# Performance work log

Measured on AMD Instinct MI355X. Metric: run time of the kernel, lower is better.

The kernel has to match this reference:

```python
import jax, jax.numpy as jnp
import numpy as np

NEG_SLOPE = 0.1
BN_EPS = 1e-5

def lrelu(z):
    return jax.nn.leaky_relu(z, NEG_SLOPE)

def conv1d(x, w, b):
    # x: [B,C,L], w: [O,I,K], 'same' padding for K=3
    y = jax.lax.conv_general_dilated(x, w, (1,), [(1, 1)], dimension_numbers=('NCH', 'OIH', 'NCH'))
    return y + b[None, :, None]

def batchnorm_train(x, g, be):
    # training-mode BatchNorm1d over (B, L) per channel; x: [B,C,L]
    m = x.mean(axis=(0, 2), keepdims=True)
    v = x.var(axis=(0, 2), keepdims=True)
    return g[None, :, None] * (x - m) * jax.lax.rsqrt(v + BN_EPS) + be[None, :, None]

def setup_inputs() -> dict:
    key = jax.random.key(0)
    ks = jax.random.split(key, 16)
    L, B, E = 100, 32, 512
    F, K, M, H, DEC = 256, 3, 128, 512, 512
    D = F + 2  # cnn feats + 2 coord dims
    s = 0.02
    inp = {
        'x': jax.random.normal(ks[0], (L, B, E), jnp.float32),
        'h': jax.random.normal(ks[1], (B, H), jnp.float32),
        'cw1': jax.random.normal(ks[2], (F, E, K), jnp.float32) * s,
        'cb1': jnp.zeros((F,), jnp.float32),
        'g1': jnp.ones((F,), jnp.float32), 'be1': jnp.zeros((F,), jnp.float32),
        'cw2': jax.random.normal(ks[3], (F, F, K), jnp.float32) * s,
        'cb2': jnp.zeros((F,), jnp.float32),
        'g2': jnp.ones((F,), jnp.float32), 'be2': jnp.zeros((F,), jnp.float32),
        'cw3': jax.random.normal(ks[4], (F, F, K), jnp.float32) * s,
        'cb3': jnp.zeros((F,), jnp.float32),
        'g3': jnp.ones((F,), jnp.float32), 'be3': jnp.zeros((F,), jnp.float32),
        'cw4': jax.random.normal(ks[5], (F, F, K), jnp.float32) * s,
        'cb4': jnp.zeros((F,), jnp.float32),
        'g4': jnp.ones((F,), jnp.float32), 'be4': jnp.zeros((F,), jnp.float32),
        'W1': jax.random.normal(ks[6], (2 * D + H, M), jnp.float32) * s,
        'b1': jnp.zeros((M,), jnp.float32),
        'W2': jax.random.normal(ks[7], (M, M), jnp.float32) * s,
        'b2': jnp.zeros((M,), jnp.float32),
        'W3': jax.random.normal(ks[8], (M, M), jnp.float32) * s,
        'b3': jnp.zeros((M,), jnp.float32),
        'W4': jax.random.normal(ks[9], (M, M), jnp.float32) * s,
        'b4': jnp.zeros((M,), jnp.float32),
        'F1': jax.random.normal(ks[10], (M, M), jnp.float32) * s,
        'fb1': jnp.zeros((M,), jnp.float32),
        'F2': jax.random.normal(ks[11], (M, DEC), jnp.float32) * s,
        'fb2': jnp.zeros((DEC,), jnp.float32),
    }
    return inp

def reference(x, h, cw1, cb1, g1, be1, cw2, cb2, g2, be2, cw3, cb3, g3, be3,
              cw4, cb4, g4, be4, W1, b1, W2, b2, W3, b3, W4, b4, F1, fb1, F2, fb2):
    # x: [L,B,E] -> [B,E,L]
    xc = jnp.transpose(x, (1, 2, 0))
    for cw, cb, g, be in ((cw1, cb1, g1, be1), (cw2, cb2, g2, be2),
                          (cw3, cb3, g3, be3), (cw4, cb4, g4, be4)):
        xc = batchnorm_train(lrelu(conv1d(xc, cw, cb)), g, be)
    xc = jnp.transpose(xc, (0, 2, 1))  # [B,L,F]
    B, L, _ = xc.shape
    # coordinate tensor: cvt_coord(i, L) = [(i/sqrt(L)-2)/2, (i%sqrt(L)-2)/2]
    i = jnp.arange(L, dtype=jnp.float32)
    sL = jnp.sqrt(jnp.float32(L))
    coord = jnp.stack([(i / sL - 2.0) / 2.0, (jnp.mod(i, sL) - 2.0) / 2.0], axis=-1)
    xf = jnp.concatenate([xc, jnp.broadcast_to(coord, (B, L, 2))], axis=-1)  # [B,L,D]
    D = xf.shape[-1]
    # pair[b,i,j] = [xf[b,j], xf[b,i], h[b]]; split W1 to avoid materializing concat
    Wa, Wb, Wc = W1[:D], W1[D:2 * D], W1[2 * D:]
    A = xf @ Wa                              # contribution of x_j, [B,L,M]
    C = xf @ Wb + (h @ Wc + b1)[:, None, :]  # contribution of x_i and h, [B,L,M]
    g = lrelu(C[:, :, None, :] + A[:, None, :, :])  # [B,L,L,M]
    g = lrelu(g @ W2 + b2)
    g = lrelu(g @ W3 + b3)
    g = lrelu(g @ W4 + b4)
    s = g.sum(axis=(1, 2))  # sum-pool over all L*L pairs -> [B,M]
    out = lrelu(lrelu(s @ F1 + fb1) @ F2 + fb2)  # [B,dec_hid]
    return out
```

## Files before the change

### kernel.cpp

```cpp
#include <hip/hip_runtime.h>
#include <hip/hip_bf16.h>
#include <stdint.h>
#include <stddef.h>

#define NEG 0.1f

typedef __attribute__((ext_vector_type(8))) short short8;
typedef __attribute__((ext_vector_type(16))) float floatx16;

__device__ __forceinline__ unsigned f2bf(float f) {
  union { float f; unsigned u; } v; v.f = f;
  unsigned r = v.u + 0x7FFFu + ((v.u >> 16) & 1u);
  return r >> 16;
}
__device__ __forceinline__ unsigned pk2bf(float a, float b) {
  __hip_bfloat162 hh = __float22bfloat162_rn(make_float2(a, b));
  union { __hip_bfloat162 h; unsigned u; } v; v.h = hh; return v.u;
}
__device__ __forceinline__ float bits2f(unsigned u) {
  union { unsigned u; float f; } v; v.u = u; return v.f;
}

__global__ void k_prep(const float* __restrict__ cw1, const float* __restrict__ cw2,
                       const float* __restrict__ cw3, const float* __restrict__ cw4,
                       unsigned short* __restrict__ wt1, unsigned short* __restrict__ wt2,
                       unsigned short* __restrict__ wt3, unsigned short* __restrict__ wt4,
                       const float* __restrict__ W1, unsigned short* __restrict__ wab,
                       const float* __restrict__ W2, const float* __restrict__ W3,
                       const float* __restrict__ W4, unsigned short* __restrict__ wmlp,
                       const float* __restrict__ h, float* __restrict__ hc) {
  __shared__ float tile[64 * 65];
  int bid = blockIdx.x, tid = threadIdx.x;
  if (bid < 1280) {
    int z = bid;
    int E; const float* cw; unsigned short* wt;
    if (z < 512) { E = 512; cw = cw1; wt = wt1; }
    else {
      int q = (z - 512) >> 8; E = 256;
      cw = (q == 0) ? cw2 : ((q == 1) ? cw3 : cw4);
      wt = (q == 0) ? wt2 : ((q == 1) ? wt3 : wt4);
      z = (z - 512) & 255;
    }
    int idx = z * 256 + tid;
    int f = idx / E, e = idx - f * E;
    const float* s = cw + (size_t)idx * 3;
    unsigned short* d = wt + (size_t)f * 3 * E + e;
    d[0] = (unsigned short)f2bf(s[0]);
    d[E] = (unsigned short)f2bf(s[1]);
    d[2 * E] = (unsigned short)f2bf(s[2]);
  } else if (bid < 1304) {
    int tw = bid - 1280;
    int half = tw / 12, rem = tw % 12, dt = rem >> 1, nt = rem & 1;
    int c = tid & 63, rq = tid >> 6;
#pragma unroll
    for (int it = 0; it < 16; ++it) {
      int r = rq + it * 4;
      int kp = dt * 64 + r;
      float v = 0.f;
      if (kp < 258) v = W1[(size_t)(half * 258 + kp) * 128 + nt * 64 + c];
      tile[r * 65 + c] = v;
    }
    __syncthreads();
#pragma unroll
    for (int it = 0; it < 16; ++it) {
      int r2 = rq + it * 4;
      wab[(size_t)(half * 128 + nt * 64 + r2) * 384 + dt * 64 + c] =
          (unsigned short)f2bf(tile[c * 65 + r2]);
    }
  } else if (bid < 1496) {
    int i2 = (bid - 1304) * 256 + tid;
    int n = i2 & 127, k = (i2 >> 7) & 127, zz = i2 >> 14;
    const float* W = (zz == 0) ? W2 : ((zz == 1) ? W3 : W4);
    float v = W[k * 128 + n];
    int w = n >> 5, l = ((k >> 3) & 1) * 32 + (n & 31), kk = k >> 4, j = k & 7;
    int i = (((zz * 4 + w) * 8 + kk) << 9) | (l << 3) | j;
    wmlp[i] = (unsigned short)f2bf(v);
  } else {
    int t = bid - 1496;
    int b = t >> 2, seg = t & 3;
    int m = tid & 127, sub = tid >> 7;
    int k0 = seg * 128 + sub * 64;
    const float* hr = h + b * 512 + k0;
    const float* Wc = W1 + (size_t)(516 + k0) * 128 + m;
    float a0 = 0.f, a1 = 0.f, a2 = 0.f, a3 = 0.f, a4 = 0.f, a5 = 0.f, a6 = 0.f, a7 = 0.f;
#pragma unroll
    for (int k = 0; k < 64; k += 8) {
      a0 += hr[k + 0] * Wc[(size_t)(k + 0) * 128];
      a1 += hr[k + 1] * Wc[(size_t)(k + 1) * 128];
      a2 += hr[k + 2] * Wc[(size_t)(k + 2) * 128];
      a3 += hr[k + 3] * Wc[(size_t)(k + 3) * 128];
      a4 += hr[k + 4] * Wc[(size_t)(k + 4) * 128];
      a5 += hr[k + 5] * Wc[(size_t)(k + 5) * 128];
      a6 += hr[k + 6] * Wc[(size_t)(k + 6) * 128];
      a7 += hr[k + 7] * Wc[(size_t)(k + 7) * 128];
    }
    float s = ((a0 + a1) + (a2 + a3)) + ((a4 + a5) + (a6 + a7));
    atomicAdd(&hc[b * 128 + m], s);
  }
}

__global__ __launch_bounds__(256, 2) void k_conv(
    const float* __restrict__ zin, const float* __restrict__ bnin,
    const float* __restrict__ gamv, const float* __restrict__ betv,
    const unsigned short* __restrict__ wt, const float* __restrict__ cb,
    float* __restrict__ zout, float* __restrict__ bnout, int E, int xmode) {
  extern __shared__ unsigned short smem[];
  const int SL = (E == 512) ? 520 : 264;
  unsigned short* slab = smem;
  unsigned short* Bs = smem + 34 * SL;
  const int K = 3 * E, NC = K >> 6, NCH = NC >> 1;
  const int esh = (E == 512) ? 9 : 8;
  int tid = threadIdx.x;
  int lane = tid & 63, wave = tid >> 6;
  int khalf = wave >> 1, cwave = wave & 1;
  int r0 = blockIdx.x * 32, ct = blockIdx.y;
  int i32 = lane & 31;
  int koff = (lane >> 5) << 3;

  int lrow = (r0 + i32) % 100;
  bool vks0 = (lrow >= 1), vks2 = (lrow <= 98);

  if (xmode) {
    for (int s = wave; s < 34; s += 4) {
      int m = r0 - 1 + s; m = min(max(m, 0), 3199);
      int b = m / 100, l = m - b * 100;
      size_t base = (size_t)(l * 32 + b) * 512;
#pragma unroll
      for (int cc = 0; cc < 2; ++cc) {
        int ch = cc * 256 + lane * 4;
        float4 v = *(const float4*)(zin + base + ch);
        uint2 p; p.x = pk2bf(v.x, v.y); p.y = pk2bf(v.z, v.w);
        *(uint2*)(&slab[s * SL + ch]) = p;
      }
    }
  } else {
    const float inv = 1.f / 3200.f;
    float sc[4], sh[4];
#pragma unroll
    for (int q = 0; q < 4; ++q) {
      int ch = lane * 4 + q;
      float mme = bnin[ch] * inv;
      float var = bnin[256 + ch] * inv - mme * mme;
      sc[q] = gamv[ch] * rsqrtf(var + 1e-5f);
      sh[q] = betv[ch] - mme * sc[q];
    }
    for (int s = wave; s < 34; s += 4) {
      int m = r0 - 1 + s; m = min(max(m, 0), 3199);
      float4 v = *(const float4*)(zin + (size_t)m * 256 + lane * 4);
      uint2 p;
      p.x = pk2bf(v.x * sc[0] + sh[0], v.y * sc[1] + sh[1]);
      p.y = pk2bf(v.z * sc[2] + sh[2], v.w * sc[3] + sh[3]);
      *(uint2*)(&slab[s * SL + lane * 4]) = p;
    }
  }

  floatx16 acc;
#pragma unroll
  for (int q = 0; q < 16; ++q) acc[q] = 0.f;

  int t128 = tid & 127;
  int brow = t128 >> 1, bhalf = (t128 & 1) * 32;
  const unsigned short* wrow = wt + (size_t)(ct * 64 + brow) * K + khalf * NCH * 64 + bhalf;
  uint4 pre[4];
#pragma unroll
  for (int t = 0; t < 4; ++t) pre[t] = *(const uint4*)(wrow + t * 8);

  for (int c = 0; c < NCH; ++c) {
    unsigned short* Bc = Bs + (khalf * 2 + (c & 1)) * (64 * 72);
#pragma unroll
    for (int t = 0; t < 4; ++t)
      *(uint4*)(&Bc[brow * 72 + bhalf + t * 8]) = pre[t];
    __syncthreads();
    if (c + 1 < NCH) {
#pragma unroll
      for (int t = 0; t < 4; ++t)
        pre[t] = *(const uint4*)(wrow + (c + 1) * 64 + t * 8);
    }
    int cg = khalf * NCH + c;
    int ks = (cg << 6) >> esh;
    int ebase = (cg << 6) & (E - 1);
    bool v = (ks == 0) ? vks0 : ((ks == 2) ? vks2 : true);
    int srow = i32 + ks;
#pragma unroll
    for (int kk = 0; kk < 4; ++kk) {
      short8 a = {};
      if (v) a = *(const short8*)(&slab[srow * SL + ebase + kk * 16 + koff]);
      short8 b8 = *(const short8*)(&Bc[(cwave * 32 + i32) * 72 + kk * 16 + koff]);
      acc = __builtin_amdgcn_mfma_f32_32x32x16_bf16(a, b8, acc, 0, 0, 0);
    }
  }

  __syncthreads();
  float* scr = (float*)smem;
  if (khalf == 1) {
#pragma unroll
    for (int reg = 0; reg < 16; ++reg) {
      int rowp = (reg & 3) + 8 * (reg >> 2) + 4 * (lane >> 5);
      scr[cwave * 1024 + rowp * 32 + i32] = acc[reg];
    }
  }
  __syncthreads();
  if (khalf == 0) {
    int f = ct * 64 + cwave * 32 + i32;
    float bias = cb[f];
    float s1 = 0.f, s2 = 0.f;
#pragma unroll
    for (int reg = 0; reg < 16; ++reg) {
      int rowp = (reg & 3) + 8 * (reg >> 2) + 4 * (lane >> 5);
      int m = r0 + rowp;
      float v = acc[reg] + scr[cwave * 1024 + rowp * 32 + i32] + bias;
      v = fmaxf(v, NEG * v);
      zout[(size_t)m * 256 + f] = v;
      s1 += v; s2 += v * v;
    }
    s1 += __shfl_xor(s1, 32, 64);
    s2 += __shfl_xor(s2, 32, 64);
    if (lane < 32) { atomicAdd(&bnout[f], s1); atomicAdd(&bnout[256 + f], s2); }
  }
}

__global__ __launch_bounds__(128, 2) void k_ac(
    const float* __restrict__ zin, const float* __restrict__ bnin,
    const float* __restrict__ gamv, const float* __restrict__ betv,
    const unsigned short* __restrict__ wab, const float* __restrict__ hc,
    const float* __restrict__ b1v,
    unsigned short* __restrict__ Abf, unsigned short* __restrict__ Cbf) {
  __shared__ unsigned short slab[32 * 328];
  __shared__ unsigned short Bs[2 * 64 * 72];
  int tid = threadIdx.x;
  int lane = tid & 63, wave = tid >> 6;
  int r0 = blockIdx.x * 32, ct = blockIdx.y;
  int i32 = lane & 31;
  int koff = (lane >> 5) << 3;
  const float inv = 1.f / 3200.f;

  {
    float sc[4], sh[4];
#pragma unroll
    for (int q = 0; q < 4; ++q) {
      int ch = lane * 4 + q;
      float mme = bnin[ch] * inv;
      float var = bnin[256 + ch] * inv - mme * mme;
      sc[q] = gamv[ch] * rsqrtf(var + 1e-5f);
      sh[q] = betv[ch] - mme * sc[q];
    }
    for (int s = wave; s < 32; s += 2) {
      int m = r0 + s;
      float4 v = *(const float4*)(zin + (size_t)m * 256 + lane * 4);
      uint2 p;
      p.x = pk2bf(v.x * sc[0] + sh[0], v.y * sc[1] + sh[1]);
      p.y = pk2bf(v.z * sc[2] + sh[2], v.w * sc[3] + sh[3]);
      *(uint2*)(&slab[s * 328 + lane * 4]) = p;
    }
    if (wave == 0) {
      int s = i32, half = (lane >> 5) * 32;
      int m = r0 + s, l = m % 100;
      float c0 = ((float)l * 0.1f - 2.0f) * 0.5f;
      float c1 = ((float)(l % 10) - 2.0f) * 0.5f;
#pragma unroll
      for (int seg = 0; seg < 4; ++seg) {
        uint4 z4; z4.x = z4.y = z4.z = z4.w = 0u;
        if (half == 0 && seg == 0) z4.x = pk2bf(c0, c1);
        *(uint4*)(&slab[s * 328 + 256 + half + seg * 8]) = z4;
      }
    }
  }

  floatx16 acc;
#pragma unroll
  for (int q = 0; q < 16; ++q) acc[q] = 0.f;

  int brow = tid >> 1, bhalf = (tid & 1) * 32;
  uint4 pre[4];
#pragma unroll
  for (int t = 0; t < 4; ++t)
    pre[t] = *(const uint4*)(wab + (size_t)(ct * 64 + brow) * 384 + bhalf + t * 8);

  for (int c = 0; c < 5; ++c) {
    unsigned short* Bc = Bs + (c & 1) * (64 * 72);
#pragma unroll
    for (int t = 0; t < 4; ++t)
      *(uint4*)(&Bc[brow * 72 + bhalf + t * 8]) = pre[t];
    __syncthreads();
    if (c + 1 < 5) {
#pragma unroll
      for (int t = 0; t < 4; ++t)
        pre[t] = *(const uint4*)(wab + (size_t)(ct * 64 + brow) * 384 + (c + 1) * 64 + bhalf + t * 8);
    }
#pragma unroll
    for (int kk = 0; kk < 4; ++kk) {
      short8 a = *(const short8*)(&slab[i32 * 328 + c * 64 + kk * 16 + koff]);
      short8 b8 = *(const short8*)(&Bc[(wave * 32 + i32) * 72 + kk * 16 + koff]);
      acc = __builtin_amdgcn_mfma_f32_32x32x16_bf16(a, b8, acc, 0, 0, 0);
    }
  }

  int n = ct * 64 + wave * 32 + i32;
#pragma unroll
  for (int reg = 0; reg < 16; ++reg) {
    int rowp = (reg & 3) + 8 * (reg >> 2) + 4 * (lane >> 5);
    int m = r0 + rowp;
    float v = acc[reg];
    if (ct < 2) {
      Abf[(size_t)m * 128 + n] = (unsigned short)f2bf(v);
    } else {
      int b = m / 100;
      int nc = n - 128;
      Cbf[(size_t)m * 128 + nc] =
          (unsigned short)f2bf(v + hc[b * 128 + nc] + b1v[nc]);
    }
  }
}

__global__ __launch_bounds__(256, 2) void k_mlp(
    const unsigned short* __restrict__ Abf, const unsigned short* __restrict__ Cbf,
    const unsigned short* __restrict__ wmlp, const float* __restrict__ b2,
    const float* __restrict__ b3, const float* __restrict__ b4,
    float* __restrict__ sout) {
  __shared__ unsigned short gs0[128 * 128];
  __shared__ unsigned short gs1[128 * 128];
  int tid = threadIdx.x, lane = tid & 63, wave = tid >> 6;
  int ln31 = lane & 31;
  int half = lane >> 5;
  int rx = ln31 & 15;

  short8 wreg[3][8];
#pragma unroll
  for (int z = 0; z < 3; ++z)
#pragma unroll
    for (int kk = 0; kk < 8; ++kk)
      wreg[z][kk] = *(const short8*)(wmlp + (size_t)(((z * 4 + wave) * 8 + kk) * 512) + lane * 8);

  int wb = wave * 32;
  float4 bq[2][4];
#pragma unroll
  for (int q = 0; q < 4; ++q) {
    bq[0][q] = *(const float4*)(b2 + wb + q * 8 + 4 * half);
    bq[1][q] = *(const float4*)(b3 + wb + q * 8 + 4 * half);
  }
  float bv4 = b4[wb + ln31];

  for (int ti = 0; ti < 2; ++ti) {
    int t = blockIdx.x + ti * 1264;
    int b = t / 79, tt = t - b * 79;
    __syncthreads();
    {
      int lr = wb + (lane >> 1);
      int hh = lane & 1;
      int lbase = lr * 128, lrx = lr & 15;
      int r = tt * 128 + lr;
      if (r > 9999) r = 9999;
      const unsigned short* Crow = Cbf + (size_t)(b * 100 + r / 100) * 128;
      const unsigned short* Arow = Abf + (size_t)(b * 100 + r % 100) * 128;
#pragma unroll
      for (int it = 0; it < 8; ++it) {
        int cc = hh * 64 + it * 8;
        uint4 c4 = *(const uint4*)(Crow + cc);
        uint4 a4 = *(const uint4*)(Arow + cc);
        unsigned cw[4] = {c4.x, c4.y, c4.z, c4.w};
        unsigned aw[4] = {a4.x, a4.y, a4.z, a4.w};
        unsigned ow[4];
#pragma unroll
        for (int q = 0; q < 4; ++q) {
          float x0 = bits2f(cw[q] << 16) + bits2f(aw[q] << 16);
          float x1 = bits2f(cw[q] & 0xFFFF0000u) + bits2f(aw[q] & 0xFFFF0000u);
          x0 = fmaxf(x0, NEG * x0);
          x1 = fmaxf(x1, NEG * x1);
          ow[q] = pk2bf(x0, x1);
        }
        uint4 o4; o4.x = ow[0]; o4.y = ow[1]; o4.z = ow[2]; o4.w = ow[3];
        *(uint4*)(&gs0[lbase + (((hh * 8 + it) ^ lrx) << 3)]) = o4;
      }
    }
    __syncthreads();

#pragma unroll
    for (int z = 0; z < 2; ++z) {
      const unsigned short* src = z ? gs1 : gs0;
      unsigned short* dst = z ? gs0 : gs1;
#pragma unroll
      for (int rg = 0; rg < 4; ++rg) {
        floatx16 acc;
#pragma unroll
        for (int q = 0; q < 16; ++q) acc[q] = 0.f;
        int rowb = (rg * 32 + ln31) * 128;
#pragma unroll
        for (int kk = 0; kk < 8; ++kk) {
          short8 g8 = *(const short8*)(&src[rowb + (((kk * 2 + half) ^ rx) << 3)]);
          acc = __builtin_amdgcn_mfma_f32_32x32x16_bf16(wreg[z][kk], g8, acc, 0, 0, 0);
        }
        int pr = rg * 32 + ln31;
        int prb = pr * 128;
#pragma unroll
        for (int q = 0; q < 4; ++q) {
          float4 bb = bq[z][q];
          float v0 = acc[q * 4 + 0] + bb.x; v0 = fmaxf(v0, NEG * v0);
          float v1 = acc[q * 4 + 1] + bb.y; v1 = fmaxf(v1, NEG * v1);
          float v2 = acc[q * 4 + 2] + bb.z; v2 = fmaxf(v2, NEG * v2);
          float v3 = acc[q * 4 + 3] + bb.w; v3 = fmaxf(v3, NEG * v3);
          uint2 p; p.x = pk2bf(v0, v1); p.y = pk2bf(v2, v3);
          *(uint2*)(&dst[prb + (((wave * 4 + q) ^ rx) << 3) + half * 4]) = p;
        }
      }
      __syncthreads();
    }

    float colsum = 0.f;
#pragma unroll
    for (int rg = 0; rg < 4; ++rg) {
      floatx16 acc;
#pragma unroll
      for (int q = 0; q < 16; ++q) acc[q] = 0.f;
      int rowb = (rg * 32 + ln31) * 128;
#pragma unroll
      for (int kk = 0; kk < 8; ++kk) {
        short8 a8 = *(const short8*)(&gs0[rowb + (((kk * 2 + half) ^ rx) << 3)]);
        acc = __builtin_amdgcn_mfma_f32_32x32x16_bf16(a8, wreg[2][kk], acc, 0, 0, 0);
      }
#pragma unroll
      for (int reg = 0; reg < 16; ++reg) {
        int rowp = (reg & 3) + 8 * (reg >> 2) + 4 * half;
        int p = tt * 128 + rg * 32 + rowp;
        float v = acc[reg] + bv4;
        v = fmaxf(v, NEG * v);
        colsum += (p < 10000) ? v : 0.f;
      }
    }
    colsum += __shfl_xor(colsum, 32, 64);
    if (lane < 32) atomicAdd(&sout[b * 128 + wb + lane], colsum);
  }
}

__global__ void k_final(const float* __restrict__ s, const float* __restrict__ F1,
                        const float* __restrict__ fb1, const float* __restrict__ F2,
                        const float* __restrict__ fb2, float* __restrict__ out) {
  __shared__ float sl[128], t1[128];
  int b = blockIdx.x, t = threadIdx.x;
  if (t < 128) sl[t] = s[b * 128 + t];
  __syncthreads();
  if (t < 128) {
    float a = fb1[t];
    for (int k = 0; k < 128; ++k) a += sl[k] * F1[k * 128 + t];
    t1[t] = fmaxf(a, NEG * a);
  }
  __syncthreads();
  for (int o = t; o < 512; o += 256) {
    float a = fb2[o];
    for (int k = 0; k < 128; ++k) a += t1[k] * F2[k * 512 + o];
    out[b * 512 + o] = fmaxf(a, NEG * a);
  }
}

extern "C" void kernel_launch(void* const* d_in, const int* in_sizes, int n_in,
                              void* d_out, int out_size, void* d_ws, size_t ws_size,
                              hipStream_t stream) {
  const float* x   = (const float*)d_in[0];
  const float* h   = (const float*)d_in[1];
  const float* cw1 = (const float*)d_in[2];
  const float* cb1 = (const float*)d_in[3];
  const float* g1  = (const float*)d_in[4];
  const float* be1 = (const float*)d_in[5];
  const float* cw2 = (const float*)d_in[6];
  const float* cb2 = (const float*)d_in[7];
  const float* g2  = (const float*)d_in[8];
  const float* be2 = (const float*)d_in[9];
  const float* cw3 = (const float*)d_in[10];
  const float* cb3 = (const float*)d_in[11];
  const float* g3  = (const float*)d_in[12];
  const float* be3 = (const float*)d_in[13];
  const float* cw4 = (const float*)d_in[14];
  const float* cb4 = (const float*)d_in[15];
  const float* g4  = (const float*)d_in[16];
  const float* be4 = (const float*)d_in[17];
  const float* W1  = (const float*)d_in[18];
  const float* b1  = (const float*)d_in[19];
  const float* W2  = (const float*)d_in[20];
  const float* b2  = (const float*)d_in[21];
  const float* W3  = (const float*)d_in[22];
  const float* b3  = (const float*)d_in[23];
  const float* W4  = (const float*)d_in[24];
  const float* b4  = (const float*)d_in[25];
  const float* F1  = (const float*)d_in[26];
  const float* fb1 = (const float*)d_in[27];
  const float* F2  = (const float*)d_in[28];
  const float* fb2 = (const float*)d_in[29];

  char* ws = (char*)d_ws;
  float* bn0  = (float*)(ws + 0);
  float* bn1  = (float*)(ws + 2048);
  float* bn2  = (float*)(ws + 4096);
  float* bn3  = (float*)(ws + 6144);
  float* sbuf = (float*)(ws + 8192);
  float* hc   = (float*)(ws + 24576);
  float* za   = (float*)(ws + 40960);
  float* zb   = (float*)(ws + 3317760);
  unsigned short* wt1  = (unsigned short*)(ws + 6594560);
  unsigned short* wt2  = (unsigned short*)(ws + 7380992);
  unsigned short* wt3  = (unsigned short*)(ws + 7774208);
  unsigned short* wt4  = (unsigned short*)(ws + 8167424);
  unsigned short* wab  = (unsigned short*)(ws + 8560640);
  unsigned short* wmlp = (unsigned short*)(ws + 8757248);
  unsigned short* Abf  = (unsigned short*)(ws + 8855552);
  unsigned short* Cbf  = (unsigned short*)(ws + 9674752);

  hipMemsetAsync(d_ws, 0, 40960, stream);

  k_prep<<<1624, 256, 0, stream>>>(cw1, cw2, cw3, cw4, wt1, wt2, wt3, wt4,
                                   W1, wab, W2, W3, W4, wmlp, h, hc);

  const int lds1 = (34 * 520 + 4 * 64 * 72) * 2;
  const int lds2 = (34 * 264 + 4 * 64 * 72) * 2;
  k_conv<<<dim3(100, 4), 256, lds1, stream>>>(x,  nullptr, nullptr, nullptr, wt1, cb1, za, bn0, 512, 1);
  k_conv<<<dim3(100, 4), 256, lds2, stream>>>(za, bn0, g1, be1, wt2, cb2, zb, bn1, 256, 0);
  k_conv<<<dim3(100, 4), 256, lds2, stream>>>(zb, bn1, g2, be2, wt3, cb3, za, bn2, 256, 0);
  k_conv<<<dim3(100, 4), 256, lds2, stream>>>(za, bn2, g3, be3, wt4, cb4, zb, bn3, 256, 0);

  k_ac<<<dim3(100, 4), 128, 0, stream>>>(zb, bn3, g4, be4, wab, hc, b1, Abf, Cbf);

  k_mlp<<<1264, 256, 0, stream>>>(Abf, Cbf, wmlp, b2, b3, b4, sbuf);
  k_final<<<32, 256, 0, stream>>>(sbuf, F1, fb1, F2, fb2, (float*)d_out);
}
```

Measured before the change: 283.6 us.

## Restructure weight prep, ping-pong MLP buffers, and split final GEMV reductions

Result: slower. 308.0 us (+8.6%).

```diff
diff --git a/kernel.cpp b/kernel.cpp
--- a/kernel.cpp
+++ b/kernel.cpp
@@ -30,27 +30,30 @@
                        const float* __restrict__ W4, unsigned short* __restrict__ wmlp,
                        const float* __restrict__ h, float* __restrict__ hc) {
   __shared__ float tile[64 * 65];
+  __shared__ unsigned short tw[1536];
   int bid = blockIdx.x, tid = threadIdx.x;
-  if (bid < 1280) {
-    int z = bid;
-    int E; const float* cw; unsigned short* wt;
-    if (z < 512) { E = 512; cw = cw1; wt = wt1; }
+  if (bid < 1024) {
+    const float* cw; unsigned short* wt; int E, f;
+    if (bid < 256) { cw = cw1; wt = wt1; E = 512; f = bid; }
     else {
-      int q = (z - 512) >> 8; E = 256;
+      int z = bid - 256; int q = z >> 8; f = z & 255; E = 256;
       cw = (q == 0) ? cw2 : ((q == 1) ? cw3 : cw4);
       wt = (q == 0) ? wt2 : ((q == 1) ? wt3 : wt4);
-      z = (z - 512) & 255;
-    }
-    int idx = z * 256 + tid;
-    int f = idx / E, e = idx - f * E;
-    const float* s = cw + (size_t)idx * 3;
-    unsigned short* d = wt + (size_t)f * 3 * E + e;
-    d[0] = (unsigned short)f2bf(s[0]);
-    d[E] = (unsigned short)f2bf(s[1]);
-    d[2 * E] = (unsigned short)f2bf(s[2]);
-  } else if (bid < 1304) {
-    int tw = bid - 1280;
-    int half = tw / 12, rem = tw % 12, dt = rem >> 1, nt = rem & 1;
+    }
+    int KE = 3 * E;
+    const float* src = cw + (size_t)f * KE;
+    for (int e = tid; e < E; e += 256) {
+      tw[e]         = (unsigned short)f2bf(src[e * 3]);
+      tw[E + e]     = (unsigned short)f2bf(src[e * 3 + 1]);
+      tw[2 * E + e] = (unsigned short)f2bf(src[e * 3 + 2]);
+    }
+    __syncthreads();
+    unsigned short* dst = wt + (size_t)f * KE;
+    int nch = KE >> 3;
+    if (tid < nch) *(uint4*)(dst + tid * 8) = *(const uint4*)(tw + tid * 8);
+  } else if (bid < 1048) {
+    int tw2 = bid - 1024;
+    int half = tw2 / 12, rem = tw2 % 12, dt = rem >> 1, nt = rem & 1;
     int c = tid & 63, rq = tid >> 6;
 #pragma unroll
     for (int it = 0; it < 16; ++it) {
@@ -67,8 +70,8 @@
       wab[(size_t)(half * 128 + nt * 64 + r2) * 384 + dt * 64 + c] =
           (unsigned short)f2bf(tile[c * 65 + r2]);
     }
-  } else if (bid < 1496) {
-    int i2 = (bid - 1304) * 256 + tid;
+  } else if (bid < 1240) {
+    int i2 = (bid - 1048) * 256 + tid;
     int n = i2 & 127, k = (i2 >> 7) & 127, zz = i2 >> 14;
     const float* W = (zz == 0) ? W2 : ((zz == 1) ? W3 : W4);
     float v = W[k * 128 + n];
@@ -76,7 +79,7 @@
     int i = (((zz * 4 + w) * 8 + kk) << 9) | (l << 3) | j;
     wmlp[i] = (unsigned short)f2bf(v);
   } else {
-    int t = bid - 1496;
+    int t = bid - 1240;
     int b = t >> 2, seg = t & 3;
     int m = tid & 127, sub = tid >> 7;
     int k0 = seg * 128 + sub * 64;
@@ -312,17 +315,105 @@
   }
 }
 
+__device__ __forceinline__ void mlp_g0(
+    unsigned short* dst, const unsigned short* __restrict__ Abf,
+    const unsigned short* __restrict__ Cbf, int b, int tt, int wave, int lane) {
+  int lr = wave * 32 + (lane >> 1);
+  int hh = lane & 1;
+  int lbase = lr * 128, lrx = lr & 15;
+  int r = tt * 128 + lr;
+  if (r > 9999) r = 9999;
+  const unsigned short* Crow = Cbf + (size_t)(b * 100 + r / 100) * 128;
+  const unsigned short* Arow = Abf + (size_t)(b * 100 + r % 100) * 128;
+#pragma unroll
+  for (int it = 0; it < 8; ++it) {
+    int cc = hh * 64 + it * 8;
+    uint4 c4 = *(const uint4*)(Crow + cc);
+    uint4 a4 = *(const uint4*)(Arow + cc);
+    unsigned cw[4] = {c4.x, c4.y, c4.z, c4.w};
+    unsigned aw[4] = {a4.x, a4.y, a4.z, a4.w};
+    unsigned ow[4];
+#pragma unroll
+    for (int q = 0; q < 4; ++q) {
+      float x0 = bits2f(cw[q] << 16) + bits2f(aw[q] << 16);
+      float x1 = bits2f(cw[q] & 0xFFFF0000u) + bits2f(aw[q] & 0xFFFF0000u);
+      x0 = fmaxf(x0, NEG * x0);
+      x1 = fmaxf(x1, NEG * x1);
+      ow[q] = pk2bf(x0, x1);
+    }
+    uint4 o4; o4.x = ow[0]; o4.y = ow[1]; o4.z = ow[2]; o4.w = ow[3];
+    *(uint4*)(&dst[lbase + (((hh * 8 + it) ^ lrx) << 3)]) = o4;
+  }
+}
+
+__device__ __forceinline__ void mlp_layerF(
+    const unsigned short* src, unsigned short* dst, const short8* wz,
+    const float4* bz, int wave, int lane) {
+  int ln31 = lane & 31, half = lane >> 5;
+  int rx = ln31 & 15;
+#pragma unroll
+  for (int rg = 0; rg < 4; ++rg) {
+    floatx16 acc;
+#pragma unroll
+    for (int q = 0; q < 16; ++q) acc[q] = 0.f;
+    int rowb = (rg * 32 + ln31) * 128;
+#pragma unroll
+    for (int kk = 0; kk < 8; ++kk) {
+      short8 g8 = *(const short8*)(&src[rowb + (((kk * 2 + half) ^ rx) << 3)]);
+      acc = __builtin_amdgcn_mfma_f32_32x32x16_bf16(wz[kk], g8, acc, 0, 0, 0);
+    }
+    int prb = (rg * 32 + ln31) * 128;
+#pragma unroll
+    for (int q = 0; q < 4; ++q) {
+      float4 bb = bz[q];
+      float v0 = acc[q * 4 + 0] + bb.x; v0 = fmaxf(v0, NEG * v0);
+      float v1 = acc[q * 4 + 1] + bb.y; v1 = fmaxf(v1, NEG * v1);
+      float v2 = acc[q * 4 + 2] + bb.z; v2 = fmaxf(v2, NEG * v2);
+      float v3 = acc[q * 4 + 3] + bb.w; v3 = fmaxf(v3, NEG * v3);
+      uint2 p; p.x = pk2bf(v0, v1); p.y = pk2bf(v2, v3);
+      *(uint2*)(&dst[prb + (((wave * 4 + q) ^ rx) << 3) + half * 4]) = p;
+    }
+  }
+}
+
+__device__ __forceinline__ float mlp_layerR(
+    const unsigned short* src, const short8* wz, float bv4, int tt, int lane) {
+  int ln31 = lane & 31, half = lane >> 5;
+  int rx = ln31 & 15;
+  float colsum = 0.f;
+#pragma unroll
+  for (int rg = 0; rg < 4; ++rg) {
+    floatx16 acc;
+#pragma unroll
+    for (int q = 0; q < 16; ++q) acc[q] = 0.f;
+    int rowb = (rg * 32 + ln31) * 128;
+#pragma unroll
+    for (int kk = 0; kk < 8; ++kk) {
+      short8 a8 = *(const short8*)(&src[rowb + (((kk * 2 + half) ^ rx) << 3)]);
+      acc = __builtin_amdgcn_mfma_f32_32x32x16_bf16(a8, wz[kk], acc, 0, 0, 0);
+    }
+#pragma unroll
+    for (int reg = 0; reg < 16; ++reg) {
+      int rowp = (reg & 3) + 8 * (reg >> 2) + 4 * half;
+      int p = tt * 128 + rg * 32 + rowp;
+      float v = acc[reg] + bv4;
+      v = fmaxf(v, NEG * v);
+      colsum += (p < 10000) ? v : 0.f;
+    }
+  }
+  return colsum;
+}
+
 __global__ __launch_bounds__(256, 2) void k_mlp(
     const unsigned short* __restrict__ Abf, const unsigned short* __restrict__ Cbf,
     const unsigned short* __restrict__ wmlp, const float* __restrict__ b2,
     const float* __restrict__ b3, const float* __restrict__ b4,
     float* __restrict__ sout) {
-  __shared__ unsigned short gs0[128 * 128];
-  __shared__ unsigned short gs1[128 * 128];
+  __shared__ unsigned short gsX[128 * 128];
+  __shared__ unsigned short gsY[128 * 128];
   int tid = threadIdx.x, lane = tid & 63, wave = tid >> 6;
-  int ln31 = lane & 31;
-  int half = lane >> 5;
-  int rx = ln31 & 15;
+  int ln31 = lane & 31, half = lane >> 5;
+  int wb = wave * 32;
 
   short8 wreg[3][8];
 #pragma unroll
@@ -331,7 +422,6 @@
     for (int kk = 0; kk < 8; ++kk)
       wreg[z][kk] = *(const short8*)(wmlp + (size_t)(((z * 4 + wave) * 8 + kk) * 512) + lane * 8);
 
-  int wb = wave * 32;
   float4 bq[2][4];
 #pragma unroll
   for (int q = 0; q < 4; ++q) {
@@ -340,113 +430,65 @@
   }
   float bv4 = b4[wb + ln31];
 
-  for (int ti = 0; ti < 2; ++ti) {
-    int t = blockIdx.x + ti * 1264;
-    int b = t / 79, tt = t - b * 79;
-    __syncthreads();
-    {
-      int lr = wb + (lane >> 1);
-      int hh = lane & 1;
-      int lbase = lr * 128, lrx = lr & 15;
-      int r = tt * 128 + lr;
-      if (r > 9999) r = 9999;
-      const unsigned short* Crow = Cbf + (size_t)(b * 100 + r / 100) * 128;
-      const unsigned short* Arow = Abf + (size_t)(b * 100 + r % 100) * 128;
-#pragma unroll
-      for (int it = 0; it < 8; ++it) {
-        int cc = hh * 64 + it * 8;
-        uint4 c4 = *(const uint4*)(Crow + cc);
-        uint4 a4 = *(const uint4*)(Arow + cc);
-        unsigned cw[4] = {c4.x, c4.y, c4.z, c4.w};
-        unsigned aw[4] = {a4.x, a4.y, a4.z, a4.w};
-        unsigned ow[4];
-#pragma unroll
-        for (int q = 0; q < 4; ++q) {
-          float x0 = bits2f(cw[q] << 16) + bits2f(aw[q] << 16);
-          float x1 = bits2f(cw[q] & 0xFFFF0000u) + bits2f(aw[q] & 0xFFFF0000u);
-          x0 = fmaxf(x0, NEG * x0);
-          x1 = fmaxf(x1, NEG * x1);
-          ow[q] = pk2bf(x0, x1);
-        }
-        uint4 o4; o4.x = ow[0]; o4.y = ow[1]; o4.z = ow[2]; o4.w = ow[3];
-        *(uint4*)(&gs0[lbase + (((hh * 8 + it) ^ lrx) << 3)]) = o4;
-      }
-    }
-    __syncthreads();
-
-#pragma unroll
-    for (int z = 0; z < 2; ++z) {
-      const unsigned short* src = z ? gs1 : gs0;
-      unsigned short* dst = z ? gs0 : gs1;
-#pragma unroll
-      for (int rg = 0; rg < 4; ++rg) {
-        floatx16 acc;
-#pragma unroll
-        for (int q = 0; q < 16; ++q) acc[q] = 0.f;
-        int rowb = (rg * 32 + ln31) * 128;
-#pragma unroll
-        for (int kk = 0; kk < 8; ++kk) {
-          short8 g8 = *(const short8*)(&src[rowb + (((kk * 2 + half) ^ rx) << 3)]);
-          acc = __builtin_amdgcn_mfma_f32_32x32x16_bf16(wreg[z][kk], g8, acc, 0, 0, 0);
-        }
-        int pr = rg * 32 + ln31;
-        int prb = pr * 128;
-#pragma unroll
-        for (int q = 0; q < 4; ++q) {
-          float4 bb = bq[z][q];
-          float v0 = acc[q * 4 + 0] + bb.x; v0 = fmaxf(v0, NEG * v0);
-          float v1 = acc[q * 4 + 1] + bb.y; v1 = fmaxf(v1, NEG * v1);
-          float v2 = acc[q * 4 + 2] + bb.z; v2 = fmaxf(v2, NEG * v2);
-          float v3 = acc[q * 4 + 3] + bb.w; v3 = fmaxf(v3, NEG * v3);
-          uint2 p; p.x = pk2bf(v0, v1); p.y = pk2bf(v2, v3);
-          *(uint2*)(&dst[prb + (((wave * 4 + q) ^ rx) << 3) + half * 4]) = p;
-        }
-      }
-      __syncthreads();
-    }
-
-    float colsum = 0.f;
-#pragma unroll
-    for (int rg = 0; rg < 4; ++rg) {
-      floatx16 acc;
-#pragma unroll
-      for (int q = 0; q < 16; ++q) acc[q] = 0.f;
-      int rowb = (rg * 32 + ln31) * 128;
-#pragma unroll
-      for (int kk = 0; kk < 8; ++kk) {
-        short8 a8 = *(const short8*)(&gs0[rowb + (((kk * 2 + half) ^ rx) << 3)]);
-        acc = __builtin_amdgcn_mfma_f32_32x32x16_bf16(a8, wreg[2][kk], acc, 0, 0, 0);
-      }
-#pragma unroll
-      for (int reg = 0; reg < 16; ++reg) {
-        int rowp = (reg & 3) + 8 * (reg >> 2) + 4 * half;
-        int p = tt * 128 + rg * 32 + rowp;
-        float v = acc[reg] + bv4;
-        v = fmaxf(v, NEG * v);
-        colsum += (p < 10000) ? v : 0.f;
-      }
-    }
-    colsum += __shfl_xor(colsum, 32, 64);
-    if (lane < 32) atomicAdd(&sout[b * 128 + wb + lane], colsum);
-  }
+  int t0 = blockIdx.x, t1 = blockIdx.x + 1264;
+  int b0 = t0 / 79, tt0 = t0 - b0 * 79;
+  int b1 = t1 / 79, tt1 = t1 - b1 * 79;
+
+  mlp_g0(gsX, Abf, Cbf, b0, tt0, wave, lane);
+  __syncthreads();
+  mlp_layerF(gsX, gsY, wreg[0], bq[0], wave, lane);
+  __syncthreads();
+  mlp_layerF(gsY, gsX, wreg[1], bq[1], wave, lane);
+  __syncthreads();
+  float cs0 = mlp_layerR(gsX, wreg[2], bv4, tt0, lane);
+  cs0 += __shfl_xor(cs0, 32, 64);
+  if (lane < 32) atomicAdd(&sout[b0 * 128 + wb + lane], cs0);
+  mlp_g0(gsY, Abf, Cbf, b1, tt1, wave, lane);
+  __syncthreads();
+  mlp_layerF(gsY, gsX, wreg[0], bq[0], wave, lane);
+  __syncthreads();
+  mlp_layerF(gsX, gsY, wreg[1], bq[1], wave, lane);
+  __syncthreads();
+  float cs1 = mlp_layerR(gsY, wreg[2], bv4, tt1, lane);
+  cs1 += __shfl_xor(cs1, 32, 64);
+  if (lane < 32) atomicAdd(&sout[b1 * 128 + wb + lane], cs1);
 }
 
 __global__ void k_final(const float* __restrict__ s, const float* __restrict__ F1,
                         const float* __restrict__ fb1, const float* __restrict__ F2,
                         const float* __restrict__ fb2, float* __restrict__ out) {
-  __shared__ float sl[128], t1[128];
+  __shared__ float sl[128], part[256], t1[128];
   int b = blockIdx.x, t = threadIdx.x;
   if (t < 128) sl[t] = s[b * 128 + t];
   __syncthreads();
+  {
+    int m = t & 127, kh = t >> 7;
+    const float* Fp = F1 + m;
+    float a0 = 0.f, a1 = 0.f, a2 = 0.f, a3 = 0.f;
+    for (int k = kh * 64; k < kh * 64 + 64; k += 4) {
+      a0 += sl[k + 0] * Fp[(size_t)(k + 0) * 128];
+      a1 += sl[k + 1] * Fp[(size_t)(k + 1) * 128];
+      a2 += sl[k + 2] * Fp[(size_t)(k + 2) * 128];
+      a3 += sl[k + 3] * Fp[(size_t)(k + 3) * 128];
+    }
+    part[t] = (a0 + a1) + (a2 + a3);
+  }
+  __syncthreads();
   if (t < 128) {
-    float a = fb1[t];
-    for (int k = 0; k < 128; ++k) a += sl[k] * F1[k * 128 + t];
+    float a = part[t] + part[t + 128] + fb1[t];
     t1[t] = fmaxf(a, NEG * a);
   }
   __syncthreads();
   for (int o = t; o < 512; o += 256) {
-    float a = fb2[o];
-    for (int k = 0; k < 128; ++k) a += t1[k] * F2[k * 512 + o];
+    const float* Fp = F2 + o;
+    float a0 = fb2[o], a1 = 0.f, a2 = 0.f, a3 = 0.f;
+    for (int k = 0; k < 128; k += 4) {
+      a0 += t1[k + 0] * Fp[(size_t)(k + 0) * 512];
+      a1 += t1[k + 1] * Fp[(size_t)(k + 1) * 512];
+      a2 += t1[k + 2] * Fp[(size_t)(k + 2) * 512];
+      a3 += t1[k + 3] * Fp[(size_t)(k + 3) * 512];
+    }
+    float a = (a0 + a1) + (a2 + a3);
     out[b * 512 + o] = fmaxf(a, NEG * a);
   }
 }
@@ -505,7 +547,7 @@
 
   hipMemsetAsync(d_ws, 0, 40960, stream);
 
-  k_prep<<<1624, 256, 0, stream>>>(cw1, cw2, cw3, cw4, wt1, wt2, wt3, wt4,
+  k_prep<<<1368, 256, 0, stream>>>(cw1, cw2, cw3, cw4, wt1, wt2, wt3, wt4,
                                    W1, wab, W2, W3, W4, wmlp, h, hc);
 
   const int lds1 = (34 * 520 + 4 * 64 * 72) * 2;
```

## Split conv into per-wave column tiles, parallelize final MLP, prefetch F1/F2

Applied to the files above, without the earlier changes.

Result: slower. 289.8 us (+2.2%).

```diff
diff --git a/kernel.cpp b/kernel.cpp
--- a/kernel.cpp
+++ b/kernel.cpp
@@ -28,7 +28,9 @@
                        const float* __restrict__ W1, unsigned short* __restrict__ wab,
                        const float* __restrict__ W2, const float* __restrict__ W3,
                        const float* __restrict__ W4, unsigned short* __restrict__ wmlp,
-                       const float* __restrict__ h, float* __restrict__ hc) {
+                       const float* __restrict__ h, float* __restrict__ hc,
+                       const float* __restrict__ F1v, const float* __restrict__ F2v,
+                       float* __restrict__ wsink) {
   __shared__ float tile[64 * 65];
   int bid = blockIdx.x, tid = threadIdx.x;
   if (bid < 1280) {
@@ -97,9 +99,17 @@
     float s = ((a0 + a1) + (a2 + a3)) + ((a4 + a5) + (a6 + a7));
     atomicAdd(&hc[b * 128 + m], s);
   }
-}
-
-__global__ __launch_bounds__(256, 2) void k_conv(
+  {
+    int wslice = bid % 80;
+    const float* wsrc = (wslice < 64) ? (F2v + (size_t)wslice * 1024)
+                                      : (F1v + (size_t)(wslice - 64) * 1024);
+    float4 v = *(const float4*)(wsrc + tid * 4);
+    float sv = v.x + v.y + v.z + v.w;
+    if (sv == 1234.5678f) wsink[0] = sv;
+  }
+}
+
+__global__ __launch_bounds__(128, 2) void k_conv(
     const float* __restrict__ zin, const float* __restrict__ bnin,
     const float* __restrict__ gamv, const float* __restrict__ betv,
     const unsigned short* __restrict__ wt, const float* __restrict__ cb,
@@ -111,8 +121,7 @@
   const int K = 3 * E, NC = K >> 6, NCH = NC >> 1;
   const int esh = (E == 512) ? 9 : 8;
   int tid = threadIdx.x;
-  int lane = tid & 63, wave = tid >> 6;
-  int khalf = wave >> 1, cwave = wave & 1;
+  int lane = tid & 63, khalf = tid >> 6;
   int r0 = blockIdx.x * 32, ct = blockIdx.y;
   int i32 = lane & 31;
   int koff = (lane >> 5) << 3;
@@ -121,7 +130,7 @@
   bool vks0 = (lrow >= 1), vks2 = (lrow <= 98);
 
   if (xmode) {
-    for (int s = wave; s < 34; s += 4) {
+    for (int s = khalf; s < 34; s += 2) {
       int m = r0 - 1 + s; m = min(max(m, 0), 3199);
       int b = m / 100, l = m - b * 100;
       size_t base = (size_t)(l * 32 + b) * 512;
@@ -144,7 +153,7 @@
       sc[q] = gamv[ch] * rsqrtf(var + 1e-5f);
       sh[q] = betv[ch] - mme * sc[q];
     }
-    for (int s = wave; s < 34; s += 4) {
+    for (int s = khalf; s < 34; s += 2) {
       int m = r0 - 1 + s; m = min(max(m, 0), 3199);
       float4 v = *(const float4*)(zin + (size_t)m * 256 + lane * 4);
       uint2 p;
@@ -153,24 +162,23 @@
       *(uint2*)(&slab[s * SL + lane * 4]) = p;
     }
   }
+  __syncthreads();
 
   floatx16 acc;
 #pragma unroll
   for (int q = 0; q < 16; ++q) acc[q] = 0.f;
 
-  int t128 = tid & 127;
-  int brow = t128 >> 1, bhalf = (t128 & 1) * 32;
-  const unsigned short* wrow = wt + (size_t)(ct * 64 + brow) * K + khalf * NCH * 64 + bhalf;
+  unsigned short* Bc = Bs + khalf * (32 * 72);
+  int brow = lane >> 1, bseg = (lane & 1) * 32;
+  const unsigned short* wrow = wt + (size_t)(ct * 32 + brow) * K + khalf * NCH * 64 + bseg;
   uint4 pre[4];
 #pragma unroll
   for (int t = 0; t < 4; ++t) pre[t] = *(const uint4*)(wrow + t * 8);
 
   for (int c = 0; c < NCH; ++c) {
-    unsigned short* Bc = Bs + (khalf * 2 + (c & 1)) * (64 * 72);
 #pragma unroll
     for (int t = 0; t < 4; ++t)
-      *(uint4*)(&Bc[brow * 72 + bhalf + t * 8]) = pre[t];
-    __syncthreads();
+      *(uint4*)(&Bc[brow * 72 + bseg + t * 8]) = pre[t];
     if (c + 1 < NCH) {
 #pragma unroll
       for (int t = 0; t < 4; ++t)
@@ -185,7 +193,7 @@
     for (int kk = 0; kk < 4; ++kk) {
       short8 a = {};
       if (v) a = *(const short8*)(&slab[srow * SL + ebase + kk * 16 + koff]);
-      short8 b8 = *(const short8*)(&Bc[(cwave * 32 + i32) * 72 + kk * 16 + koff]);
+      short8 b8 = *(const short8*)(&Bc[i32 * 72 + kk * 16 + koff]);
       acc = __builtin_amdgcn_mfma_f32_32x32x16_bf16(a, b8, acc, 0, 0, 0);
     }
   }
@@ -196,19 +204,19 @@
 #pragma unroll
     for (int reg = 0; reg < 16; ++reg) {
       int rowp = (reg & 3) + 8 * (reg >> 2) + 4 * (lane >> 5);
-      scr[cwave * 1024 + rowp * 32 + i32] = acc[reg];
+      scr[rowp * 32 + i32] = acc[reg];
     }
   }
   __syncthreads();
   if (khalf == 0) {
-    int f = ct * 64 + cwave * 32 + i32;
+    int f = ct * 32 + i32;
     float bias = cb[f];
     float s1 = 0.f, s2 = 0.f;
 #pragma unroll
     for (int reg = 0; reg < 16; ++reg) {
       int rowp = (reg & 3) + 8 * (reg >> 2) + 4 * (lane >> 5);
       int m = r0 + rowp;
-      float v = acc[reg] + scr[cwave * 1024 + rowp * 32 + i32] + bias;
+      float v = acc[reg] + scr[rowp * 32 + i32] + bias;
       v = fmaxf(v, NEG * v);
       zout[(size_t)m * 256 + f] = v;
       s1 += v; s2 += v * v;
@@ -290,7 +298,7 @@
 #pragma unroll
     for (int kk = 0; kk < 4; ++kk) {
       short8 a = *(const short8*)(&slab[i32 * 328 + c * 64 + kk * 16 + koff]);
-      short8 b8 = *(const short8*)(&Bc[(wave * 32 + i32) * 72 + kk * 16 + koff]);
+      short8 b8 = *(const short8*)(&Bs[(c & 1) * (64 * 72) + (wave * 32 + i32) * 72 + kk * 16 + koff]);
       acc = __builtin_amdgcn_mfma_f32_32x32x16_bf16(a, b8, acc, 0, 0, 0);
     }
   }
@@ -389,8 +397,7 @@
           short8 g8 = *(const short8*)(&src[rowb + (((kk * 2 + half) ^ rx) << 3)]);
           acc = __builtin_amdgcn_mfma_f32_32x32x16_bf16(wreg[z][kk], g8, acc, 0, 0, 0);
         }
-        int pr = rg * 32 + ln31;
-        int prb = pr * 128;
+        int prb = (rg * 32 + ln31) * 128;
 #pragma unroll
         for (int q = 0; q < 4; ++q) {
           float4 bb = bq[z][q];
@@ -434,19 +441,39 @@
 __global__ void k_final(const float* __restrict__ s, const float* __restrict__ F1,
                         const float* __restrict__ fb1, const float* __restrict__ F2,
                         const float* __restrict__ fb2, float* __restrict__ out) {
-  __shared__ float sl[128], t1[128];
+  __shared__ float sl[128], part[512], t1[128];
   int b = blockIdx.x, t = threadIdx.x;
   if (t < 128) sl[t] = s[b * 128 + t];
   __syncthreads();
+  {
+    int m = t & 127, kh = t >> 7;
+    const float* Fp = F1 + m;
+    float a0 = 0.f, a1 = 0.f, a2 = 0.f, a3 = 0.f;
+    for (int k = kh * 32; k < kh * 32 + 32; k += 4) {
+      a0 += sl[k + 0] * Fp[(size_t)(k + 0) * 128];
+      a1 += sl[k + 1] * Fp[(size_t)(k + 1) * 128];
+      a2 += sl[k + 2] * Fp[(size_t)(k + 2) * 128];
+      a3 += sl[k + 3] * Fp[(size_t)(k + 3) * 128];
+    }
+    part[t] = (a0 + a1) + (a2 + a3);
+  }
+  __syncthreads();
   if (t < 128) {
-    float a = fb1[t];
-    for (int k = 0; k < 128; ++k) a += sl[k] * F1[k * 128 + t];
+    float a = (part[t] + part[t + 128]) + (part[t + 256] + part[t + 384]) + fb1[t];
     t1[t] = fmaxf(a, NEG * a);
   }
   __syncthreads();
-  for (int o = t; o < 512; o += 256) {
-    float a = fb2[o];
-    for (int k = 0; k < 128; ++k) a += t1[k] * F2[k * 512 + o];
+  {
+    int o = t;
+    const float* Fp = F2 + o;
+    float a0 = fb2[o], a1 = 0.f, a2 = 0.f, a3 = 0.f;
+    for (int k = 0; k < 128; k += 4) {
+      a0 += t1[k + 0] * Fp[(size_t)(k + 0) * 512];
+      a1 += t1[k + 1] * Fp[(size_t)(k + 1) * 512];
+      a2 += t1[k + 2] * Fp[(size_t)(k + 2) * 512];
+      a3 += t1[k + 3] * Fp[(size_t)(k + 3) * 512];
+    }
+    float a = (a0 + a1) + (a2 + a3);
     out[b * 512 + o] = fmaxf(a, NEG * a);
   }
 }
@@ -502,21 +529,22 @@
   unsigned short* wmlp = (unsigned short*)(ws + 8757248);
   unsigned short* Abf  = (unsigned short*)(ws + 8855552);
   unsigned short* Cbf  = (unsigned short*)(ws + 9674752);
+  float* wsink = (float*)(ws + 10493952);
 
   hipMemsetAsync(d_ws, 0, 40960, stream);
 
   k_prep<<<1624, 256, 0, stream>>>(cw1, cw2, cw3, cw4, wt1, wt2, wt3, wt4,
-                                   W1, wab, W2, W3, W4, wmlp, h, hc);
-
-  const int lds1 = (34 * 520 + 4 * 64 * 72) * 2;
-  const int lds2 = (34 * 264 + 4 * 64 * 72) * 2;
-  k_conv<<<dim3(100, 4), 256, lds1, stream>>>(x,  nullptr, nullptr, nullptr, wt1, cb1, za, bn0, 512, 1);
-  k_conv<<<dim3(100, 4), 256, lds2, stream>>>(za, bn0, g1, be1, wt2, cb2, zb, bn1, 256, 0);
-  k_conv<<<dim3(100, 4), 256, lds2, stream>>>(zb, bn1, g2, be2, wt3, cb3, za, bn2, 256, 0);
-  k_conv<<<dim3(100, 4), 256, lds2, stream>>>(za, bn2, g3, be3, wt4, cb4, zb, bn3, 256, 0);
+                                   W1, wab, W2, W3, W4, wmlp, h, hc, F1, F2, wsink);
+
+  const int lds1 = (34 * 520 + 2 * 32 * 72) * 2;
+  const int lds2 = (34 * 264 + 2 * 32 * 72) * 2;
+  k_conv<<<dim3(100, 8), 128, lds1, stream>>>(x,  nullptr, nullptr, nullptr, wt1, cb1, za, bn0, 512, 1);
+  k_conv<<<dim3(100, 8), 128, lds2, stream>>>(za, bn0, g1, be1, wt2, cb2, zb, bn1, 256, 0);
+  k_conv<<<dim3(100, 8), 128, lds2, stream>>>(zb, bn1, g2, be2, wt3, cb3, za, bn2, 256, 0);
+  k_conv<<<dim3(100, 8), 128, lds2, stream>>>(za, bn2, g3, be3, wt4, cb4, zb, bn3, 256, 0);
 
   k_ac<<<dim3(100, 4), 128, 0, stream>>>(zb, bn3, g4, be4, wab, hc, b1, Abf, Cbf);
 
   k_mlp<<<1264, 256, 0, stream>>>(Abf, Cbf, wmlp, b2, b3, b4, sbuf);
-  k_final<<<32, 256, 0, stream>>>(sbuf, F1, fb1, F2, fb2, (float*)d_out);
-}
+  k_final<<<32, 512, 0, stream>>>(sbuf, F1, fb1, F2, fb2, (float*)d_out);
+}
```
